# Kernel tuning notes

Measured on AMD Instinct MI355X. Metric: run time of the kernel, lower is better.

Reference implementation:

```python
import jax, jax.numpy as jnp
import numpy as np

KERNEL_SIZE = 3
ITERATIONS = 4


def _box_conv(x, kernel):
    # x: [B,1,H,W], kernel: [1,1,k,k]; SAME padding via pad=(k-1)//2
    p = (KERNEL_SIZE - 1) // 2
    return jax.lax.conv_general_dilated(
        x, kernel,
        window_strides=(1, 1),
        padding=((p, p), (p, p)),
        dimension_numbers=("NCHW", "OIHW", "NCHW"),
    )


def setup_inputs() -> dict:
    key = jax.random.key(0)
    inputs = jax.random.uniform(key, (32, 1, 512, 512), dtype=jnp.float32)
    return {"inputs": inputs}


def reference(inputs) -> jnp.ndarray:
    # fixed box-filter kernel: every tap = 1/k^2, bias = 0 (frozen in torch module)
    kernel = jnp.full((1, 1, KERNEL_SIZE, KERNEL_SIZE), 1.0 / KERNEL_SIZE**2, dtype=inputs.dtype)
    blob = inputs
    for _ in range(ITERATIONS):
        # NOTE: original module convolves `inputs` (not previous blob) each iteration
        blob = _box_conv(inputs, kernel)
        blob = jax.nn.sigmoid((blob - 0.01) * 1000.0)
        blob = _box_conv(blob, kernel)
        blob = jax.nn.sigmoid((blob - 0.9) * 1000.0)
    return blob
```

## Files before the change

kernel.cpp:

```cpp
#include <hip/hip_runtime.h>


#define IMG 512
#define NB  32

#define TX 64
#define TY 32
#define RX 68
#define RY 36
#define RXP 72
#define SX 66
#define SY 34
#define SXP 68

__device__ __forceinline__ float steep_sig(float sum9, float bias) {
    float x = fmaf(sum9, 1000.0f / 9.0f, bias);
    float e = __expf(-x);
    return __builtin_amdgcn_rcpf(1.0f + e);
}

__global__ __launch_bounds__(256, 4) void blobber_fused(
        const float* __restrict__ in, float* __restrict__ out) {
    __shared__ float sIn[RY][RXP];
    __shared__ float sS1[SY][SXP];

    const int tid = threadIdx.x;
    const int tx  = tid & 63;
    const int tyg = tid >> 6;
    const int x0  = blockIdx.x * TX;
    const int y0  = blockIdx.y * TY;

    const float* img  = in  + (size_t)blockIdx.z * (IMG * IMG);
    float*       oimg = out + (size_t)blockIdx.z * (IMG * IMG);

    #pragma unroll
    for (int iy = tyg; iy < RY; iy += 4) {
        int gy = y0 - 2 + iy;
        bool rowok = (unsigned)gy < IMG;
        const float* row = img + gy * IMG;
        int gx = x0 - 2 + tx;
        sIn[iy][tx] = (rowok && (unsigned)gx < IMG) ? row[gx] : 0.0f;
        if (tx < 4) {
            int gx2 = gx + 64;
            sIn[iy][tx + 64] = (rowok && (unsigned)gx2 < IMG) ? row[gx2] : 0.0f;
        }
    }
    __syncthreads();

    #pragma unroll
    for (int iy = tyg; iy < SY; iy += 4) {
        int gy = y0 - 1 + iy;
        bool rowok = (unsigned)gy < IMG;
        {
            int sx = tx;
            int gx = x0 - 1 + sx;
            float t = 0.0f;
            #pragma unroll
            for (int dy = 0; dy < 3; ++dy)
                t += sIn[iy + dy][sx] + sIn[iy + dy][sx + 1] + sIn[iy + dy][sx + 2];
            sS1[iy][sx] = (rowok && (unsigned)gx < IMG) ? steep_sig(t, -10.0f) : 0.0f;
        }
        if (tx < 2) {
            int sx = 64 + tx;
            int gx = x0 - 1 + sx;
            float t = 0.0f;
            #pragma unroll
            for (int dy = 0; dy < 3; ++dy)
                t += sIn[iy + dy][sx] + sIn[iy + dy][sx + 1] + sIn[iy + dy][sx + 2];
            sS1[iy][sx] = (rowok && (unsigned)gx < IMG) ? steep_sig(t, -10.0f) : 0.0f;
        }
    }
    __syncthreads();

    #pragma unroll
    for (int oy = tyg; oy < TY; oy += 4) {
        float t = 0.0f;
        #pragma unroll
        for (int dy = 0; dy < 3; ++dy)
            t += sS1[oy + dy][tx] + sS1[oy + dy][tx + 1] + sS1[oy + dy][tx + 2];
        oimg[(y0 + oy) * IMG + x0 + tx] = steep_sig(t, -900.0f);
    }
}

extern "C" void kernel_launch(void* const* d_in, const int* in_sizes, int n_in,
                              void* d_out, int out_size, void* d_ws, size_t ws_size,
                              hipStream_t stream) {
    const float* in  = (const float*)d_in[0];
    float*       out = (float*)d_out;
    dim3 grid(IMG / TX, IMG / TY, NB);
    blobber_fused<<<grid, 256, 0, stream>>>(in, out);
}
```

Before: 98.82 us.

## Vectorize box-filter stages with float4 and separable row/column sums

Rewrites the fused kernel so it loads and stores with float4 vectors and splits each 3x3 box sum into separate vertical and horizontal passes held in extra shared-memory buffers. The aim is fewer redundant adds and fewer scalar LDS and global transactions. In exchange it adds two more __syncthreads barriers, more shared memory per block that may lower occupancy, and a halo load of 4 columns per side instead of 2.

```diff
diff --git a/kernel.cpp b/kernel.cpp
--- a/kernel.cpp
+++ b/kernel.cpp
@@ -3,15 +3,17 @@
 
 #define IMG 512
 #define NB  32
+#define TX  64
+#define TY  32
 
-#define TX 64
-#define TY 32
-#define RX 68
-#define RY 36
-#define RXP 72
-#define SX 66
-#define SY 34
-#define SXP 68
+__device__ __forceinline__ float4 f4add3(float4 a, float4 b, float4 c) {
+    float4 r;
+    r.x = a.x + b.x + c.x;
+    r.y = a.y + b.y + c.y;
+    r.z = a.z + b.z + c.z;
+    r.w = a.w + b.w + c.w;
+    return r;
+}
 
 __device__ __forceinline__ float steep_sig(float sum9, float bias) {
     float x = fmaf(sum9, 1000.0f / 9.0f, bias);
@@ -21,64 +23,80 @@
 
 __global__ __launch_bounds__(256, 4) void blobber_fused(
         const float* __restrict__ in, float* __restrict__ out) {
-    __shared__ float sIn[RY][RXP];
-    __shared__ float sS1[SY][SXP];
+    __shared__ float4 sIn[TY + 4][18];
+    __shared__ float4 sV1[TY + 2][20];
+    __shared__ float4 sS1[TY + 2][18];
+    __shared__ float4 sH2[TY + 2][16];
 
     const int tid = threadIdx.x;
-    const int tx  = tid & 63;
-    const int tyg = tid >> 6;
     const int x0  = blockIdx.x * TX;
     const int y0  = blockIdx.y * TY;
-
     const float* img  = in  + (size_t)blockIdx.z * (IMG * IMG);
     float*       oimg = out + (size_t)blockIdx.z * (IMG * IMG);
 
-    #pragma unroll
-    for (int iy = tyg; iy < RY; iy += 4) {
-        int gy = y0 - 2 + iy;
-        bool rowok = (unsigned)gy < IMG;
-        const float* row = img + gy * IMG;
-        int gx = x0 - 2 + tx;
-        sIn[iy][tx] = (rowok && (unsigned)gx < IMG) ? row[gx] : 0.0f;
-        if (tx < 4) {
-            int gx2 = gx + 64;
-            sIn[iy][tx + 64] = (rowok && (unsigned)gx2 < IMG) ? row[gx2] : 0.0f;
-        }
+    for (int it = tid; it < (TY + 4) * 18; it += 256) {
+        int r = it / 18;
+        int q = it - r * 18;
+        int gy = y0 - 2 + r;
+        int gx = x0 - 4 + 4 * q;
+        float4 v = make_float4(0.f, 0.f, 0.f, 0.f);
+        if ((unsigned)gy < IMG && (unsigned)gx < IMG)
+            v = *(const float4*)(img + gy * IMG + gx);
+        sIn[r][q] = v;
+    }
+    for (int it = tid; it < (TY + 2) * 2; it += 256) {
+        int r = it >> 1;
+        sV1[r][(it & 1) * 19] = make_float4(0.f, 0.f, 0.f, 0.f);
     }
     __syncthreads();
 
-    #pragma unroll
-    for (int iy = tyg; iy < SY; iy += 4) {
-        int gy = y0 - 1 + iy;
-        bool rowok = (unsigned)gy < IMG;
-        {
-            int sx = tx;
-            int gx = x0 - 1 + sx;
-            float t = 0.0f;
-            #pragma unroll
-            for (int dy = 0; dy < 3; ++dy)
-                t += sIn[iy + dy][sx] + sIn[iy + dy][sx + 1] + sIn[iy + dy][sx + 2];
-            sS1[iy][sx] = (rowok && (unsigned)gx < IMG) ? steep_sig(t, -10.0f) : 0.0f;
-        }
-        if (tx < 2) {
-            int sx = 64 + tx;
-            int gx = x0 - 1 + sx;
-            float t = 0.0f;
-            #pragma unroll
-            for (int dy = 0; dy < 3; ++dy)
-                t += sIn[iy + dy][sx] + sIn[iy + dy][sx + 1] + sIn[iy + dy][sx + 2];
-            sS1[iy][sx] = (rowok && (unsigned)gx < IMG) ? steep_sig(t, -10.0f) : 0.0f;
-        }
+    for (int it = tid; it < (TY + 2) * 18; it += 256) {
+        int r = it / 18;
+        int q = it - r * 18;
+        sV1[r][q + 1] = f4add3(sIn[r][q], sIn[r + 1][q], sIn[r + 2][q]);
     }
     __syncthreads();
 
-    #pragma unroll
-    for (int oy = tyg; oy < TY; oy += 4) {
-        float t = 0.0f;
-        #pragma unroll
-        for (int dy = 0; dy < 3; ++dy)
-            t += sS1[oy + dy][tx] + sS1[oy + dy][tx + 1] + sS1[oy + dy][tx + 2];
-        oimg[(y0 + oy) * IMG + x0 + tx] = steep_sig(t, -900.0f);
+    for (int it = tid; it < (TY + 2) * 18; it += 256) {
+        int r = it / 18;
+        int j = it - r * 18;
+        int gy = y0 - 1 + r;
+        int gx = x0 - 4 + 4 * j;
+        float4 s = make_float4(0.f, 0.f, 0.f, 0.f);
+        if ((unsigned)gy < IMG && (unsigned)gx < IMG) {
+            float4 A = sV1[r][j], B = sV1[r][j + 1], C = sV1[r][j + 2];
+            s.x = steep_sig(A.w + B.x + B.y, -10.0f);
+            s.y = steep_sig(B.x + B.y + B.z, -10.0f);
+            s.z = steep_sig(B.y + B.z + B.w, -10.0f);
+            s.w = steep_sig(B.z + B.w + C.x, -10.0f);
+        }
+        sS1[r][j] = s;
+    }
+    __syncthreads();
+
+    for (int it = tid; it < (TY + 2) * 16; it += 256) {
+        int r = it >> 4;
+        int m = it & 15;
+        float4 A = sS1[r][m], B = sS1[r][m + 1], C = sS1[r][m + 2];
+        float4 h;
+        h.x = A.w + B.x + B.y;
+        h.y = B.x + B.y + B.z;
+        h.z = B.y + B.z + B.w;
+        h.w = B.z + B.w + C.x;
+        sH2[r][m] = h;
+    }
+    __syncthreads();
+
+    for (int it = tid; it < TY * 16; it += 256) {
+        int r = it >> 4;
+        int m = it & 15;
+        float4 a = sH2[r][m], b = sH2[r + 1][m], c = sH2[r + 2][m];
+        float4 o;
+        o.x = steep_sig(a.x + b.x + c.x, -900.0f);
+        o.y = steep_sig(a.y + b.y + c.y, -900.0f);
+        o.z = steep_sig(a.z + b.z + c.z, -900.0f);
+        o.w = steep_sig(a.w + b.w + c.w, -900.0f);
+        *(float4*)(oimg + (y0 + r) * IMG + x0 + 4 * m) = o;
     }
 }
 
```

Measured after the change: 90.33 us. 8.6% less time.

## Replace shared-memory tiles with per-wave register row bands and shuffles

Applied to the files above, without the earlier changes.

Each wavefront now handles one full 512-wide row band of 8 output rows, holding input rows as float4 registers. Horizontal neighbours are exchanged with wave shuffles and vertical sums roll through registers, which removes shared memory and block barriers. Loads and stores become 128-bit vectorised. The band halo is smaller relative to tile size than the old 64x32 tiles, but it brings more register pressure, serial dependence down the band and fewer independent blocks (512 blocks of 4 waves).

```diff
diff --git a/kernel.cpp b/kernel.cpp
--- a/kernel.cpp
+++ b/kernel.cpp
@@ -2,83 +2,116 @@
 
 
 #define IMG 512
-#define NB  32
-
-#define TX 64
-#define TY 32
-#define RX 68
-#define RY 36
-#define RXP 72
-#define SX 66
-#define SY 34
-#define SXP 68
+#define BH  8
+#define NROWS (BH + 4)
+#define NIT   (BH + 2)
 
 __device__ __forceinline__ float steep_sig(float sum9, float bias) {
     float x = fmaf(sum9, 1000.0f / 9.0f, bias);
-    float e = __expf(-x);
-    return __builtin_amdgcn_rcpf(1.0f + e);
+    return __builtin_amdgcn_rcpf(1.0f + __expf(-x));
 }
 
-__global__ __launch_bounds__(256, 4) void blobber_fused(
-        const float* __restrict__ in, float* __restrict__ out) {
-    __shared__ float sIn[RY][RXP];
-    __shared__ float sS1[SY][SXP];
+__device__ __forceinline__ float4 f4add3(float4 a, float4 b, float4 c) {
+    return make_float4(a.x + b.x + c.x, a.y + b.y + c.y,
+                       a.z + b.z + c.z, a.w + b.w + c.w);
+}
 
-    const int tid = threadIdx.x;
-    const int tx  = tid & 63;
-    const int tyg = tid >> 6;
-    const int x0  = blockIdx.x * TX;
-    const int y0  = blockIdx.y * TY;
+__global__ __launch_bounds__(256) void blobber_fused(const float* __restrict__ in,
+                                                     float* __restrict__ out) {
+    const int tid  = threadIdx.x;
+    const int lane = tid & 63;
+    const int gw   = blockIdx.x * 4 + (tid >> 6);
+    const int band = gw & 63;
+    const int img  = gw >> 6;
+    const int y0   = band * BH;
 
-    const float* img  = in  + (size_t)blockIdx.z * (IMG * IMG);
-    float*       oimg = out + (size_t)blockIdx.z * (IMG * IMG);
+    const int colL = 4 * lane;
+    const int colR = 256 + 4 * lane;
+
+    const float* ip = in  + (size_t)img * (IMG * IMG);
+    float*       op = out + (size_t)img * (IMG * IMG);
+
+    float4 inL[NROWS], inR[NROWS];
+    #pragma unroll
+    for (int k = 0; k < NROWS; ++k) {
+        const int r = y0 - 2 + k;
+        inL[k] = make_float4(0.f, 0.f, 0.f, 0.f);
+        inR[k] = make_float4(0.f, 0.f, 0.f, 0.f);
+        if ((unsigned)r < IMG) {
+            inL[k] = *(const float4*)(ip + r * IMG + colL);
+            inR[k] = *(const float4*)(ip + r * IMG + colR);
+        }
+    }
+
+    const float4 z4 = make_float4(0.f, 0.f, 0.f, 0.f);
+    float4 h2mL = z4, h2cL = z4, h2mR = z4, h2cR = z4;
 
     #pragma unroll
-    for (int iy = tyg; iy < RY; iy += 4) {
-        int gy = y0 - 2 + iy;
-        bool rowok = (unsigned)gy < IMG;
-        const float* row = img + gy * IMG;
-        int gx = x0 - 2 + tx;
-        sIn[iy][tx] = (rowok && (unsigned)gx < IMG) ? row[gx] : 0.0f;
-        if (tx < 4) {
-            int gx2 = gx + 64;
-            sIn[iy][tx + 64] = (rowok && (unsigned)gx2 < IMG) ? row[gx2] : 0.0f;
+    for (int s = 0; s < NIT; ++s) {
+        const int r = y0 - 1 + s;
+
+        float4 vL = f4add3(inL[s], inL[s + 1], inL[s + 2]);
+        float4 vR = f4add3(inR[s], inR[s + 1], inR[s + 2]);
+
+        float Llft = __shfl_up(vL.w, 1);
+        float Lrgt = __shfl_down(vL.x, 1);
+        float Rlft = __shfl_up(vR.w, 1);
+        float Rrgt = __shfl_down(vR.x, 1);
+        float c256 = __shfl(vR.x, 0);
+        float c255 = __shfl(vL.w, 63);
+        if (lane == 0)  { Llft = 0.0f;  Rlft = c255; }
+        if (lane == 63) { Lrgt = c256;  Rrgt = 0.0f; }
+
+        float4 s1L, s1R;
+        if ((unsigned)r < IMG) {
+            s1L.x = steep_sig(Llft + vL.x + vL.y, -10.0f);
+            s1L.y = steep_sig(vL.x + vL.y + vL.z, -10.0f);
+            s1L.z = steep_sig(vL.y + vL.z + vL.w, -10.0f);
+            s1L.w = steep_sig(vL.z + vL.w + Lrgt, -10.0f);
+            s1R.x = steep_sig(Rlft + vR.x + vR.y, -10.0f);
+            s1R.y = steep_sig(vR.x + vR.y + vR.z, -10.0f);
+            s1R.z = steep_sig(vR.y + vR.z + vR.w, -10.0f);
+            s1R.w = steep_sig(vR.z + vR.w + Rrgt, -10.0f);
+        } else {
+            s1L = z4; s1R = z4;
         }
-    }
-    __syncthreads();
 
-    #pragma unroll
-    for (int iy = tyg; iy < SY; iy += 4) {
-        int gy = y0 - 1 + iy;
-        bool rowok = (unsigned)gy < IMG;
-        {
-            int sx = tx;
-            int gx = x0 - 1 + sx;
-            float t = 0.0f;
-            #pragma unroll
-            for (int dy = 0; dy < 3; ++dy)
-                t += sIn[iy + dy][sx] + sIn[iy + dy][sx + 1] + sIn[iy + dy][sx + 2];
-            sS1[iy][sx] = (rowok && (unsigned)gx < IMG) ? steep_sig(t, -10.0f) : 0.0f;
+        float sLl = __shfl_up(s1L.w, 1);
+        float sLr = __shfl_down(s1L.x, 1);
+        float sRl = __shfl_up(s1R.w, 1);
+        float sRr = __shfl_down(s1R.x, 1);
+        float s256 = __shfl(s1R.x, 0);
+        float s255 = __shfl(s1L.w, 63);
+        if (lane == 0)  { sLl = 0.0f;  sRl = s255; }
+        if (lane == 63) { sLr = s256;  sRr = 0.0f; }
+
+        float4 h2pL, h2pR;
+        h2pL.x = sLl   + s1L.x + s1L.y;
+        h2pL.y = s1L.x + s1L.y + s1L.z;
+        h2pL.z = s1L.y + s1L.z + s1L.w;
+        h2pL.w = s1L.z + s1L.w + sLr;
+        h2pR.x = sRl   + s1R.x + s1R.y;
+        h2pR.y = s1R.x + s1R.y + s1R.z;
+        h2pR.z = s1R.y + s1R.z + s1R.w;
+        h2pR.w = s1R.z + s1R.w + sRr;
+
+        if (s >= 2) {
+            const int oy = r - 1;
+            float4 oL, oR;
+            oL.x = steep_sig(h2mL.x + h2cL.x + h2pL.x, -900.0f);
+            oL.y = steep_sig(h2mL.y + h2cL.y + h2pL.y, -900.0f);
+            oL.z = steep_sig(h2mL.z + h2cL.z + h2pL.z, -900.0f);
+            oL.w = steep_sig(h2mL.w + h2cL.w + h2pL.w, -900.0f);
+            oR.x = steep_sig(h2mR.x + h2cR.x + h2pR.x, -900.0f);
+            oR.y = steep_sig(h2mR.y + h2cR.y + h2pR.y, -900.0f);
+            oR.z = steep_sig(h2mR.z + h2cR.z + h2pR.z, -900.0f);
+            oR.w = steep_sig(h2mR.w + h2cR.w + h2pR.w, -900.0f);
+            *(float4*)(op + oy * IMG + colL) = oL;
+            *(float4*)(op + oy * IMG + colR) = oR;
         }
-        if (tx < 2) {
-            int sx = 64 + tx;
-            int gx = x0 - 1 + sx;
-            float t = 0.0f;
-            #pragma unroll
-            for (int dy = 0; dy < 3; ++dy)
-                t += sIn[iy + dy][sx] + sIn[iy + dy][sx + 1] + sIn[iy + dy][sx + 2];
-            sS1[iy][sx] = (rowok && (unsigned)gx < IMG) ? steep_sig(t, -10.0f) : 0.0f;
-        }
-    }
-    __syncthreads();
 
-    #pragma unroll
-    for (int oy = tyg; oy < TY; oy += 4) {
-        float t = 0.0f;
-        #pragma unroll
-        for (int dy = 0; dy < 3; ++dy)
-            t += sS1[oy + dy][tx] + sS1[oy + dy][tx + 1] + sS1[oy + dy][tx + 2];
-        oimg[(y0 + oy) * IMG + x0 + tx] = steep_sig(t, -900.0f);
+        h2mL = h2cL; h2cL = h2pL;
+        h2mR = h2cR; h2cR = h2pR;
     }
 }
 
@@ -87,6 +120,5 @@
                               hipStream_t stream) {
     const float* in  = (const float*)d_in[0];
     float*       out = (float*)d_out;
-    dim3 grid(IMG / TX, IMG / TY, NB);
-    blobber_fused<<<grid, 256, 0, stream>>>(in, out);
+    blobber_fused<<<dim3(512), dim3(256), 0, stream>>>(in, out);
 }
```

New measurement: 83.91 us. 1.18x faster.
